# Optimization experiments

Measured on AMD Instinct MI355X. Metric: run time of the kernel, lower is better.

Reference implementation:

```python
import jax, jax.numpy as jnp
import numpy as np

S, B, H, D, IN = 512, 8, 8, 64, 512  # seq, batch, heads, head dim, model dim
PROJ = H * (5 * D + 2)


def setup_inputs() -> dict:
    key = jax.random.key(0)
    k0, k1, k2 = jax.random.split(key, 3)
    x = jax.random.normal(k0, (S, B, IN), jnp.float32)
    W_slow = jax.random.normal(k1, (PROJ, IN), jnp.float32) / np.sqrt(IN).astype(np.float32)
    W_out = jax.random.normal(k2, (IN, H * D), jnp.float32) / np.sqrt(H * D).astype(np.float32)
    ln_gamma = jnp.ones((IN,), jnp.float32)
    ln_beta = jnp.zeros((IN,), jnp.float32)
    return dict(x=x, W_slow=W_slow, W_out=W_out, ln_gamma=ln_gamma, ln_beta=ln_beta)


def reference(x, W_slow, W_out, ln_gamma, ln_beta):
    slen, bsz, in_dim = x.shape
    # pre-LayerNorm (torch LayerNorm: biased variance, eps=1e-5)
    mu = x.mean(-1, keepdims=True)
    var = x.var(-1, keepdims=True)
    normed = (x - mu) / jnp.sqrt(var + 1e-5) * ln_gamma + ln_beta
    qkvb = (normed @ W_slow.T).reshape(slen, bsz, H, 5 * D + 2)
    q, k, v, rk, rv, beta, rbeta = jnp.split(
        qkvb, [D, 2 * D, 3 * D, 4 * D, 5 * D, 5 * D + 1], axis=-1)
    q = jax.nn.softmax(q, axis=-1)
    k = jax.nn.softmax(k, axis=-1)
    rk = jax.nn.softmax(rk, axis=-1)
    beta = jax.nn.sigmoid(beta)    # (S,B,H,1)
    rbeta = jax.nn.sigmoid(rbeta)  # (S,B,H,1)

    # ---- fast_weight_memory: delta-rule fast weight, z_t = W_t q_t ----
    W0 = jnp.zeros((bsz, H, D, D), x.dtype)

    def fw_step(W, inp):
        qt, kt, vt, bt = inp  # (B,H,D),(B,H,D),(B,H,D),(B,H,1)
        v_old = jnp.einsum('bhij,bhj->bhi', W, kt)
        W = W + (bt * (vt - v_old))[..., :, None] * kt[..., None, :]
        z = jnp.einsum('bhij,bhj->bhi', W, qt)
        return W, z

    _, z = jax.lax.scan(fw_step, W0, (q, k, v, beta))  # z: (S,B,H,D)

    # ---- fast_rnn_v2: recurrent fast weight, h_t = z_t + R_t softmax(h_{t-1}) ----
    R0 = jnp.zeros((bsz, H, D, D), x.dtype)
    h0 = jnp.zeros((bsz, H, D), x.dtype)

    def rec_step(carry, inp):
        R, h = carry
        zt, kt, vt, bt = inp
        qh = jax.nn.softmax(h, axis=-1)
        v_old = jnp.einsum('bhij,bhj->bhi', R, kt)
        R = R + (bt * (vt - v_old))[..., :, None] * kt[..., None, :]
        h = zt + jnp.einsum('bhij,bhj->bhi', R, qh)
        return (R, h), h

    _, hs = jax.lax.scan(rec_step, (R0, h0), (z, rk, rv, rbeta))  # (S,B,H,D)

    out = hs.reshape(slen, bsz, H * D) @ W_out.T  # (S,B,IN)
    # dropout = 0.0 -> identity; residual
    return x + out
```

## Files before the change

### kernel.cpp

```cpp
#include <hip/hip_runtime.h>

#define S_LEN 512
#define BSZ 8
#define NH 8
#define HD 64
#define IN_DIM 512
#define PROJ 2576
#define SEG 322
#define AST 352
#define CHUNK 8
#define NCH 64
#define CB (CHUNK * AST * 4)

typedef __attribute__((ext_vector_type(8))) __bf16 bf16x8;
typedef __attribute__((ext_vector_type(4))) float f32x4;

static __device__ __forceinline__ unsigned short f2bf(float f) {
  unsigned u = __float_as_uint(f);
  unsigned r = (u + 0x7fffu + ((u >> 16) & 1u)) >> 16;
  return (unsigned short)r;
}
static __device__ __forceinline__ float bf2f(unsigned short s) {
  return __uint_as_float(((unsigned)s) << 16);
}

static __device__ __forceinline__ void gl_lds16(const void* g, void* l) {
  __builtin_amdgcn_global_load_lds(
      (const __attribute__((address_space(1))) unsigned int*)g,
      (__attribute__((address_space(3))) unsigned int*)l, 16, 0, 0);
}

__global__ __launch_bounds__(256) void ln_kernel(const float* __restrict__ x,
                                                 const float* __restrict__ gamma,
                                                 const float* __restrict__ beta,
                                                 unsigned short* __restrict__ out) {
  int wave = threadIdx.x >> 6, lane = threadIdx.x & 63;
  int row = blockIdx.x * 4 + wave;
  const float* xr = x + (size_t)row * IN_DIM + lane * 8;
  float4 a = *(const float4*)xr;
  float4 b = *(const float4*)(xr + 4);
  float vals[8] = {a.x, a.y, a.z, a.w, b.x, b.y, b.z, b.w};
  float s = 0.f, ss = 0.f;
#pragma unroll
  for (int i = 0; i < 8; i++) { s += vals[i]; ss += vals[i] * vals[i]; }
#pragma unroll
  for (int o = 32; o; o >>= 1) { s += __shfl_xor(s, o); ss += __shfl_xor(ss, o); }
  float mu = s * (1.f / 512.f);
  float var = ss * (1.f / 512.f) - mu * mu;
  float rstd = rsqrtf(var + 1e-5f);
  const float* g = gamma + lane * 8;
  const float* be = beta + lane * 8;
  float4 g1 = *(const float4*)g, g2 = *(const float4*)(g + 4);
  float4 b1 = *(const float4*)be, b2 = *(const float4*)(be + 4);
  float gs[8] = {g1.x, g1.y, g1.z, g1.w, g2.x, g2.y, g2.z, g2.w};
  float bs[8] = {b1.x, b1.y, b1.z, b1.w, b2.x, b2.y, b2.z, b2.w};
  union { unsigned short u[8]; uint4 v; } pk;
#pragma unroll
  for (int i = 0; i < 8; i++) pk.u[i] = f2bf((vals[i] - mu) * rstd * gs[i] + bs[i]);
  *(uint4*)(out + (size_t)row * IN_DIM + lane * 8) = pk.v;
}

__global__ void cast_kernel(const float* __restrict__ in, unsigned short* __restrict__ out, int n) {
  int i = blockIdx.x * blockDim.x + threadIdx.x;
  int st = gridDim.x * blockDim.x;
  for (; i < n; i += st) out[i] = f2bf(in[i]);
}

template <int BF16_OUT, int RESID>
__global__ __launch_bounds__(256) void gemm128(const unsigned short* __restrict__ A,
                                               const unsigned short* __restrict__ B,
                                               void* __restrict__ Cout,
                                               const float* __restrict__ resid,
                                               int M, int N, int K) {
  __shared__ __align__(16) unsigned short As[128 * 32];
  __shared__ __align__(16) unsigned short Bs[128 * 32];
  int tid = threadIdx.x;
  int lane = tid & 63, w = tid >> 6;
  int wr = w >> 1, wc = w & 1;
  int m0 = blockIdx.y * 128, n0 = blockIdx.x * 128;

  int r0 = (w * 2) * 16 + (lane >> 2);
  int r1 = (w * 2 + 1) * 16 + (lane >> 2);
  int kq = (lane & 3) * 8;
  const unsigned short* A0 = A + (size_t)(m0 + r0) * K + kq;
  const unsigned short* A1 = A + (size_t)(m0 + r1) * K + kq;
  int bn0 = n0 + r0; if (bn0 > N - 1) bn0 = N - 1;
  int bn1 = n0 + r1; if (bn1 > N - 1) bn1 = N - 1;
  const unsigned short* B0 = B + (size_t)bn0 * K + kq;
  const unsigned short* B1 = B + (size_t)bn1 * K + kq;
  char* asb0 = (char*)As + (w * 2) * 1024;
  char* asb1 = (char*)As + (w * 2 + 1) * 1024;
  char* bsb0 = (char*)Bs + (w * 2) * 1024;
  char* bsb1 = (char*)Bs + (w * 2 + 1) * 1024;

  f32x4 acc[4][4];
#pragma unroll
  for (int i = 0; i < 4; i++)
#pragma unroll
    for (int j = 0; j < 4; j++) acc[i][j] = (f32x4){0.f, 0.f, 0.f, 0.f};

  int q = lane >> 4, m16 = lane & 15;
  for (int k0 = 0; k0 < K; k0 += 32) {
    gl_lds16(A0 + k0, asb0);
    gl_lds16(A1 + k0, asb1);
    gl_lds16(B0 + k0, bsb0);
    gl_lds16(B1 + k0, bsb1);
    asm volatile("s_waitcnt vmcnt(0)" ::: "memory");
    __syncthreads();
    bf16x8 af[4], bfv[4];
#pragma unroll
    for (int f = 0; f < 4; f++)
      af[f] = *(const bf16x8*)&As[(wr * 64 + f * 16 + m16) * 32 + q * 8];
#pragma unroll
    for (int f = 0; f < 4; f++)
      bfv[f] = *(const bf16x8*)&Bs[(wc * 64 + f * 16 + m16) * 32 + q * 8];
#pragma unroll
    for (int fa = 0; fa < 4; fa++)
#pragma unroll
      for (int fb = 0; fb < 4; fb++)
        acc[fa][fb] = __builtin_amdgcn_mfma_f32_16x16x32_bf16(af[fa], bfv[fb], acc[fa][fb], 0, 0, 0);
    __syncthreads();
  }

#pragma unroll
  for (int fa = 0; fa < 4; fa++) {
#pragma unroll
    for (int fb = 0; fb < 4; fb++) {
#pragma unroll
      for (int rr = 0; rr < 4; rr++) {
        int gm = m0 + wr * 64 + fa * 16 + q * 4 + rr;
        int gn = n0 + wc * 64 + fb * 16 + m16;
        if (gn < N) {
          float v = acc[fa][fb][rr];
          if (BF16_OUT) {
            ((unsigned short*)Cout)[(size_t)gm * N + gn] = f2bf(v);
          } else {
            float o = v;
            if (RESID) o += resid[(size_t)gm * N + gn];
            ((float*)Cout)[(size_t)gm * N + gn] = o;
          }
        }
      }
    }
  }
}

__global__ __launch_bounds__(256) void act_kernel(const unsigned short* __restrict__ qkvb,
                                                  float* __restrict__ act) {
  int gw = blockIdx.x * 4 + (threadIdx.x >> 6);
  int l = threadIdx.x & 63;
  int m = gw >> 3, hh = gw & 7;
  int t = m >> 3, b = m & 7;
  const unsigned short* src = qkvb + (size_t)m * PROJ + hh * SEG;
  float fq = bf2f(src[l]);
  float fk = bf2f(src[64 + l]);
  float fv = bf2f(src[128 + l]);
  float fr = bf2f(src[192 + l]);
  float frv = bf2f(src[256 + l]);
  float mq = fq, mk = fk, mr = fr;
#pragma unroll
  for (int o = 32; o; o >>= 1) {
    mq = fmaxf(mq, __shfl_xor(mq, o));
    mk = fmaxf(mk, __shfl_xor(mk, o));
    mr = fmaxf(mr, __shfl_xor(mr, o));
  }
  float eq = __expf(fq - mq), ek = __expf(fk - mk), er = __expf(fr - mr);
  float sq = eq, sk = ek, sr = er;
#pragma unroll
  for (int o = 32; o; o >>= 1) {
    sq += __shfl_xor(sq, o);
    sk += __shfl_xor(sk, o);
    sr += __shfl_xor(sr, o);
  }
  int bh = b * 8 + hh;
  float* dst = act + ((size_t)bh * S_LEN + t) * AST;
  dst[l] = eq * __builtin_amdgcn_rcpf(sq);
  dst[64 + l] = ek * __builtin_amdgcn_rcpf(sk);
  dst[128 + l] = er * __builtin_amdgcn_rcpf(sr);
  dst[192 + l] = fv;
  dst[256 + l] = frv;
  if (l < 2) {
    float xv = bf2f(src[320 + l]);
    dst[320 + l] = __builtin_amdgcn_rcpf(1.f + __expf(-xv));
  }
}

__global__ __launch_bounds__(128, 1) void scan_kernel(const float* __restrict__ act,
                                                      unsigned short* __restrict__ hs) {
  int bh = blockIdx.x;
  int b = bh >> 3, hh = bh & 7;
  int tid = threadIdx.x, l = tid & 63, w = tid >> 6;

  __shared__ __align__(16) float stage[4][CHUNK * AST];
  __shared__ __align__(16) float zring[4][CHUNK][64];
  __shared__ __align__(16) float ehb[64];
  __shared__ int flags[16];

  volatile int* w0done = &flags[0];
  volatile int* w1done = &flags[8];

  const char* abase = (const char*)(act + (size_t)bh * S_LEN * AST);

  if (tid == 0) { flags[0] = 0; flags[8] = 0; }
  if (w) ehb[l] = 1.f;
  if (w == 0) {
#pragma unroll
    for (int i = 0; i < 11; i++)
      gl_lds16(abase + (size_t)i * 1024 + l * 16, (char*)&stage[0][0] + i * 1024);
  }
  __syncthreads();

  f32x4 M[16];
#pragma unroll
  for (int j = 0; j < 16; j++) M[j] = (f32x4){0.f, 0.f, 0.f, 0.f};
  const f32x4 z4 = {0.f, 0.f, 0.f, 0.f};

  if (w == 0) {
    for (int c = 0; c < NCH; c++) {
      if (c >= 3) {
        while (*w1done < c - 2) __builtin_amdgcn_s_sleep(2);
      }
      if (c + 1 < NCH) {
        const char* nb = abase + (size_t)(c + 1) * CB;
        char* sb = (char*)&stage[(c + 1) & 3][0];
#pragma unroll
        for (int i = 0; i < 11; i++)
          gl_lds16(nb + (size_t)i * 1024 + l * 16, sb + i * 1024);
        asm volatile("s_waitcnt vmcnt(11)" ::: "memory");
      } else {
        asm volatile("s_waitcnt vmcnt(0)" ::: "memory");
      }
      const float* cb = &stage[c & 3][0];
      float* zc = &zring[c & 3][0][0];
#pragma unroll
      for (int s = 0; s < CHUNK; s++) {
        const float* stf = cb + s * AST;
        const f32x4* st4 = (const f32x4*)stf;
        float cv = stf[192 + l];
        f32x4 kk[16];
#pragma unroll
        for (int j = 0; j < 16; j++) kk[j] = st4[16 + j];
        f32x4 a0 = z4, a1 = z4, a2 = z4, a3 = z4;
#pragma unroll
        for (int j = 0; j < 16; j += 4) {
          a0 += M[j] * kk[j];
          a1 += M[j + 1] * kk[j + 1];
          a2 += M[j + 2] * kk[j + 2];
          a3 += M[j + 3] * kk[j + 3];
        }
        f32x4 vo = (a0 + a1) + (a2 + a3);
        float vold = (vo.x + vo.y) + (vo.z + vo.w);
        float bt = stf[320];
        float coef = bt * (cv - vold);
        f32x4 c4 = {coef, coef, coef, coef};
        a0 = a1 = a2 = a3 = z4;
#pragma unroll
        for (int j = 0; j < 16; j += 4) {
          M[j] += c4 * kk[j];         a0 += M[j] * st4[j];
          M[j + 1] += c4 * kk[j + 1]; a1 += M[j + 1] * st4[j + 1];
          M[j + 2] += c4 * kk[j + 2]; a2 += M[j + 2] * st4[j + 2];
          M[j + 3] += c4 * kk[j + 3]; a3 += M[j + 3] * st4[j + 3];
        }
        vo = (a0 + a1) + (a2 + a3);
        zc[s * 64 + l] = (vo.x + vo.y) + (vo.z + vo.w);
      }
      asm volatile("s_waitcnt lgkmcnt(0)" ::: "memory");
      *w0done = c + 1;
    }
  } else {
    unsigned short* hdst = hs + (size_t)b * 512 + hh * 64 + l;
    for (int c = 0; c < NCH; c++) {
      while (*w0done < c + 1) __builtin_amdgcn_s_sleep(2);
      const float* cb = &stage[c & 3][0];
      const float* zc = &zring[c & 3][0][0];
#pragma unroll
      for (int s = 0; s < CHUNK; s++) {
        const float* stf = cb + s * AST;
        const f32x4* st4 = (const f32x4*)stf;
        float z = zc[s * 64 + l];
        float cv = stf[256 + l];
        f32x4 kk[16];
#pragma unroll
        for (int j = 0; j < 16; j++) kk[j] = st4[32 + j];
        f32x4 a0 = z4, a1 = z4, a2 = z4, a3 = z4;
#pragma unroll
        for (int j = 0; j < 16; j += 4) {
          a0 += M[j] * kk[j];
          a1 += M[j + 1] * kk[j + 1];
          a2 += M[j + 2] * kk[j + 2];
          a3 += M[j + 3] * kk[j + 3];
        }
        f32x4 vo = (a0 + a1) + (a2 + a3);
        float rvold = (vo.x + vo.y) + (vo.z + vo.w);
        float rb = stf[321];
        float rcoef = rb * (cv - rvold);
        f32x4 c4 = {rcoef, rcoef, rcoef, rcoef};
        const f32x4* e4 = (const f32x4*)ehb;
        f32x4 s0 = z4, s1 = z4, s2v = z4, s3 = z4;
        a0 = a1 = a2 = a3 = z4;
#pragma unroll
        for (int j = 0; j < 16; j += 4) {
          f32x4 e0 = e4[j], e1 = e4[j + 1], e2 = e4[j + 2], e3 = e4[j + 3];
          M[j] += c4 * kk[j];         a0 += M[j] * e0;       s0 += e0;
          M[j + 1] += c4 * kk[j + 1]; a1 += M[j + 1] * e1;   s1 += e1;
          M[j + 2] += c4 * kk[j + 2]; a2 += M[j + 2] * e2;   s2v += e2;
          M[j + 3] += c4 * kk[j + 3]; a3 += M[j + 3] * e3;   s3 += e3;
        }
        f32x4 ho = (a0 + a1) + (a2 + a3);
        f32x4 so = (s0 + s1) + (s2v + s3);
        float hp = (ho.x + ho.y) + (ho.z + ho.w);
        float sm = (so.x + so.y) + (so.z + so.w);
        float h = z + hp * __builtin_amdgcn_rcpf(sm);
        hdst[(size_t)(c * CHUNK + s) * (BSZ * 512)] = f2bf(h);
        ehb[l] = __expf(h - 20.f);
      }
      asm volatile("s_waitcnt lgkmcnt(0)" ::: "memory");
      *w1done = c + 1;
    }
  }
}

extern "C" void kernel_launch(void* const* d_in, const int* in_sizes, int n_in,
                              void* d_out, int out_size, void* d_ws, size_t ws_size,
                              hipStream_t stream) {
  const float* x = (const float*)d_in[0];
  const float* W_slow = (const float*)d_in[1];
  const float* W_out = (const float*)d_in[2];
  const float* gamma = (const float*)d_in[3];
  const float* beta = (const float*)d_in[4];

  char* ws = (char*)d_ws;
  size_t off = 0;
  unsigned short* normed = (unsigned short*)(ws + off); off += (size_t)4096 * 512 * 2;
  unsigned short* Wslow_b = (unsigned short*)(ws + off); off += (size_t)PROJ * 512 * 2;
  unsigned short* Wout_b = (unsigned short*)(ws + off); off += (size_t)512 * 512 * 2;
  unsigned short* qkvb = (unsigned short*)(ws + off); off += (size_t)4096 * PROJ * 2;
  float* act = (float*)(ws + off); off += (size_t)64 * S_LEN * AST * 4;
  unsigned short* hsb = normed;

  hipLaunchKernelGGL(ln_kernel, dim3(1024), dim3(256), 0, stream, x, gamma, beta, normed);
  hipLaunchKernelGGL(cast_kernel, dim3(512), dim3(256), 0, stream, W_slow, Wslow_b, PROJ * 512);
  hipLaunchKernelGGL(cast_kernel, dim3(256), dim3(256), 0, stream, W_out, Wout_b, 512 * 512);
  hipLaunchKernelGGL((gemm128<1, 0>), dim3((PROJ + 127) / 128, 4096 / 128), dim3(256), 0, stream,
                     normed, Wslow_b, (void*)qkvb, (const float*)nullptr, 4096, PROJ, 512);
  hipLaunchKernelGGL(act_kernel, dim3(8192), dim3(256), 0, stream, qkvb, act);
  hipLaunchKernelGGL(scan_kernel, dim3(64), dim3(128), 0, stream, act, hsb);
  hipLaunchKernelGGL((gemm128<0, 1>), dim3(512 / 128, 4096 / 128), dim3(256), 0, stream,
                     hsb, Wout_b, d_out, x, 4096, 512, 512);
}
```

Before: 402.2 us.

## Split fast-weight and recurrent scans into separate workgroups synced via global flags

The two scan stages, which previously ran as two waves in one workgroup sharing LDS, now run as separate single-wave workgroups on different CUs. They hand off z through a global buffer and per-head release/acquire flags, which are reset inside the layernorm kernel. Each workgroup streams its own activation chunks with double buffering. The goal is to give each serial recurrence a full CU and to remove the LDS ring coupling. The cost is global-memory round trips for z and flag polling latency, and correctness depends on both workgroups of a pair being co-resident.

```diff
diff --git a/kernel.cpp b/kernel.cpp
--- a/kernel.cpp
+++ b/kernel.cpp
@@ -33,7 +33,9 @@
 __global__ __launch_bounds__(256) void ln_kernel(const float* __restrict__ x,
                                                  const float* __restrict__ gamma,
                                                  const float* __restrict__ beta,
-                                                 unsigned short* __restrict__ out) {
+                                                 unsigned short* __restrict__ out,
+                                                 int* __restrict__ flags) {
+  if (blockIdx.x == 0 && threadIdx.x < 64) flags[threadIdx.x] = 0;
   int wave = threadIdx.x >> 6, lane = threadIdx.x & 63;
   int row = blockIdx.x * 4 + wave;
   const float* xr = x + (size_t)row * IN_DIM + lane * 8;
@@ -185,53 +187,45 @@
   }
 }
 
-__global__ __launch_bounds__(128, 1) void scan_kernel(const float* __restrict__ act,
-                                                      unsigned short* __restrict__ hs) {
-  int bh = blockIdx.x;
+__global__ __launch_bounds__(64, 1) void scan_kernel(const float* __restrict__ act,
+                                                     unsigned short* __restrict__ hs,
+                                                     float* __restrict__ zg,
+                                                     int* __restrict__ flags) {
+  int bid = blockIdx.x;
+  int role = bid >> 6;
+  int bh = bid & 63;
   int b = bh >> 3, hh = bh & 7;
-  int tid = threadIdx.x, l = tid & 63, w = tid >> 6;
-
-  __shared__ __align__(16) float stage[4][CHUNK * AST];
-  __shared__ __align__(16) float zring[4][CHUNK][64];
+  int l = threadIdx.x;
+
+  __shared__ __align__(16) float stage[2][CHUNK * AST];
   __shared__ __align__(16) float ehb[64];
-  __shared__ int flags[16];
-
-  volatile int* w0done = &flags[0];
-  volatile int* w1done = &flags[8];
 
   const char* abase = (const char*)(act + (size_t)bh * S_LEN * AST);
-
-  if (tid == 0) { flags[0] = 0; flags[8] = 0; }
-  if (w) ehb[l] = 1.f;
-  if (w == 0) {
-#pragma unroll
-    for (int i = 0; i < 11; i++)
-      gl_lds16(abase + (size_t)i * 1024 + l * 16, (char*)&stage[0][0] + i * 1024);
-  }
-  __syncthreads();
+  float* zb = zg + (size_t)bh * S_LEN * 64;
+
+#pragma unroll
+  for (int i = 0; i < 11; i++)
+    gl_lds16(abase + (size_t)i * 1024 + l * 16, (char*)&stage[0][0] + i * 1024);
+  asm volatile("s_waitcnt vmcnt(0)" ::: "memory");
 
   f32x4 M[16];
 #pragma unroll
   for (int j = 0; j < 16; j++) M[j] = (f32x4){0.f, 0.f, 0.f, 0.f};
   const f32x4 z4 = {0.f, 0.f, 0.f, 0.f};
 
-  if (w == 0) {
+  if (role == 0) {
     for (int c = 0; c < NCH; c++) {
-      if (c >= 3) {
-        while (*w1done < c - 2) __builtin_amdgcn_s_sleep(2);
-      }
+      asm volatile("s_waitcnt vmcnt(8)" ::: "memory");
       if (c + 1 < NCH) {
         const char* nb = abase + (size_t)(c + 1) * CB;
-        char* sb = (char*)&stage[(c + 1) & 3][0];
+        char* sb = (char*)&stage[(c + 1) & 1][0];
+        asm volatile("" ::: "memory");
 #pragma unroll
         for (int i = 0; i < 11; i++)
           gl_lds16(nb + (size_t)i * 1024 + l * 16, sb + i * 1024);
-        asm volatile("s_waitcnt vmcnt(11)" ::: "memory");
-      } else {
-        asm volatile("s_waitcnt vmcnt(0)" ::: "memory");
-      }
-      const float* cb = &stage[c & 3][0];
-      float* zc = &zring[c & 3][0][0];
+        asm volatile("" ::: "memory");
+      }
+      const float* cb = &stage[c & 1][0];
 #pragma unroll
       for (int s = 0; s < CHUNK; s++) {
         const float* stf = cb + s * AST;
@@ -262,22 +256,36 @@
           M[j + 3] += c4 * kk[j + 3]; a3 += M[j + 3] * st4[j + 3];
         }
         vo = (a0 + a1) + (a2 + a3);
-        zc[s * 64 + l] = (vo.x + vo.y) + (vo.z + vo.w);
-      }
-      asm volatile("s_waitcnt lgkmcnt(0)" ::: "memory");
-      *w0done = c + 1;
+        zb[(size_t)(c * CHUNK + s) * 64 + l] = (vo.x + vo.y) + (vo.z + vo.w);
+      }
+      asm volatile("s_waitcnt vmcnt(0)" ::: "memory");
+      if (l == 0)
+        __hip_atomic_store(&flags[bh], c + 1, __ATOMIC_RELEASE, __HIP_MEMORY_SCOPE_AGENT);
     }
   } else {
+    ehb[l] = 1.f;
     unsigned short* hdst = hs + (size_t)b * 512 + hh * 64 + l;
     for (int c = 0; c < NCH; c++) {
-      while (*w0done < c + 1) __builtin_amdgcn_s_sleep(2);
-      const float* cb = &stage[c & 3][0];
-      const float* zc = &zring[c & 3][0][0];
+      asm volatile("s_waitcnt vmcnt(16)" ::: "memory");
+      while (__hip_atomic_load(&flags[bh], __ATOMIC_ACQUIRE, __HIP_MEMORY_SCOPE_AGENT) < c + 1)
+        __builtin_amdgcn_s_sleep(8);
+      if (c + 1 < NCH) {
+        const char* nb = abase + (size_t)(c + 1) * CB;
+        char* sb = (char*)&stage[(c + 1) & 1][0];
+        asm volatile("" ::: "memory");
+#pragma unroll
+        for (int i = 0; i < 11; i++)
+          gl_lds16(nb + (size_t)i * 1024 + l * 16, sb + i * 1024);
+        asm volatile("" ::: "memory");
+      }
+      float zv[CHUNK];
+#pragma unroll
+      for (int s = 0; s < CHUNK; s++) zv[s] = zb[(size_t)(c * CHUNK + s) * 64 + l];
+      const float* cb = &stage[c & 1][0];
 #pragma unroll
       for (int s = 0; s < CHUNK; s++) {
         const float* stf = cb + s * AST;
         const f32x4* st4 = (const f32x4*)stf;
-        float z = zc[s * 64 + l];
         float cv = stf[256 + l];
         f32x4 kk[16];
 #pragma unroll
@@ -310,12 +318,10 @@
         f32x4 so = (s0 + s1) + (s2v + s3);
         float hp = (ho.x + ho.y) + (ho.z + ho.w);
         float sm = (so.x + so.y) + (so.z + so.w);
-        float h = z + hp * __builtin_amdgcn_rcpf(sm);
+        float h = zv[s] + hp * __builtin_amdgcn_rcpf(sm);
         hdst[(size_t)(c * CHUNK + s) * (BSZ * 512)] = f2bf(h);
         ehb[l] = __expf(h - 20.f);
       }
-      asm volatile("s_waitcnt lgkmcnt(0)" ::: "memory");
-      *w1done = c + 1;
     }
   }
 }
@@ -336,15 +342,17 @@
   unsigned short* Wout_b = (unsigned short*)(ws + off); off += (size_t)512 * 512 * 2;
   unsigned short* qkvb = (unsigned short*)(ws + off); off += (size_t)4096 * PROJ * 2;
   float* act = (float*)(ws + off); off += (size_t)64 * S_LEN * AST * 4;
+  float* zg = (float*)(ws + off); off += (size_t)64 * S_LEN * 64 * 4;
+  int* flags = (int*)(ws + off); off += 256;
   unsigned short* hsb = normed;
 
-  hipLaunchKernelGGL(ln_kernel, dim3(1024), dim3(256), 0, stream, x, gamma, beta, normed);
+  hipLaunchKernelGGL(ln_kernel, dim3(1024), dim3(256), 0, stream, x, gamma, beta, normed, flags);
   hipLaunchKernelGGL(cast_kernel, dim3(512), dim3(256), 0, stream, W_slow, Wslow_b, PROJ * 512);
   hipLaunchKernelGGL(cast_kernel, dim3(256), dim3(256), 0, stream, W_out, Wout_b, 512 * 512);
   hipLaunchKernelGGL((gemm128<1, 0>), dim3((PROJ + 127) / 128, 4096 / 128), dim3(256), 0, stream,
                      normed, Wslow_b, (void*)qkvb, (const float*)nullptr, 4096, PROJ, 512);
   hipLaunchKernelGGL(act_kernel, dim3(8192), dim3(256), 0, stream, qkvb, act);
-  hipLaunchKernelGGL(scan_kernel, dim3(64), dim3(128), 0, stream, act, hsb);
+  hipLaunchKernelGGL(scan_kernel, dim3(128), dim3(64), 0, stream, act, hsb, zg, flags);
   hipLaunchKernelGGL((gemm128<0, 1>), dim3(512 / 128, 4096 / 128), dim3(256), 0, stream,
                      hsb, Wout_b, d_out, x, 4096, 512, 512);
 }
```

After: 420.8 us. +4.6%, slower.
